# Performance work log

Hardware: AMD Instinct MI355X
Metric: run time of the kernel (lower is better)

The kernel has to match this reference:

```python
import jax, jax.numpy as jnp
import numpy as np

N_NODES = 100000
N_EDGES = 1000000
D_FEAT = 64
N_COARSE = 25000


def setup_inputs() -> dict:
    key = jax.random.key(0)
    k1, k2, k3 = jax.random.split(key, 3)
    x = jax.random.normal(k1, (N_NODES, D_FEAT), dtype=jnp.float32)
    edge_index = jax.random.randint(k2, (2, N_EDGES), 0, N_COARSE, dtype=jnp.int64)
    edge_attr = jax.random.uniform(k3, (N_EDGES,), dtype=jnp.float32)
    return {"x": x, "edge_index": edge_index, "edge_attr": edge_attr, "n_coarse": N_COARSE}


def reference(x, edge_index, edge_attr, n_coarse):
    # CustomPoolingAdd: for each edge e, out[dst[e]] += edge_attr[e] * x[src[e]]
    src = edge_index[0]  # [E]
    dst = edge_index[1]  # [E]
    msgs = x[src] * edge_attr[:, None]  # [E, D] gather + weight
    out = jax.ops.segment_sum(msgs, dst, num_segments=n_coarse)  # [n_coarse, D]
    return out
```

## Files before the change

kernel.cpp:

```cpp
#include <hip/hip_runtime.h>
#include <cmath>


constexpr int D4    = 16;
constexpr int NBSH  = 6;
constexpr int RPB   = 64;
constexpr int NB_LIM = 400;
constexpr int P1_C  = 3072;
constexpr int P1_K  = 19;
constexpr int CAPB  = 3072;

__global__ void __launch_bounds__(256) p1_bin_kernel(
    const int* __restrict__ src, const int* __restrict__ dst,
    const float* __restrict__ attr, int* __restrict__ cursor,
    int2* __restrict__ pairs, int n_edges, int nb) {
  __shared__ int2 bins[NB_LIM * P1_K];
  __shared__ int  bcnt[NB_LIM];
  __shared__ int  gbase_s[NB_LIM];
  for (int i = threadIdx.x; i < nb; i += 256) bcnt[i] = 0;
  __syncthreads();

  int base = blockIdx.x * P1_C;
  for (int i = threadIdx.x; i < P1_C; i += 256) {
    int e = base + i;
    if (e >= n_edges) break;
    int d = dst[e];
    int b = d >> NBSH;
    int2 pr = make_int2(src[e] | ((d & (RPB - 1)) << 24), __float_as_int(attr[e]));
    int p = atomicAdd(&bcnt[b], 1);
    if (p < P1_K) {
      bins[b * P1_K + p] = pr;
    } else {
      int g = atomicAdd(&cursor[b], 1);
      if (g < CAPB) pairs[(size_t)b * CAPB + g] = pr;
    }
  }
  __syncthreads();

  for (int b = threadIdx.x; b < nb; b += 256) {
    int c = min(bcnt[b], P1_K);
    gbase_s[b] = (c > 0) ? atomicAdd(&cursor[b], c) : 0;
  }
  __syncthreads();

  int wv = threadIdx.x >> 6, ln = threadIdx.x & 63;
  for (int b = wv; b < nb; b += 4) {
    int c = min(bcnt[b], P1_K);
    if (ln < c) {
      int g = gbase_s[b] + ln;
      if (g < CAPB) pairs[(size_t)b * CAPB + g] = bins[b * P1_K + ln];
    }
  }
}

__global__ void __launch_bounds__(512) p2_sort_kernel(
    const int* __restrict__ cursor, int2* __restrict__ pairs,
    int* __restrict__ row_off, int* __restrict__ row_cnt, int n_rows) {
  __shared__ int2 raw[CAPB];
  __shared__ int2 srt[CAPB];
  __shared__ int  cnt[RPB], off[RPB], cur[RPB];

  int b = blockIdx.x;
  int n = min(cursor[b], CAPB);
  size_t gbase = (size_t)b * CAPB;

  if (threadIdx.x < RPB) { cnt[threadIdx.x] = 0; cur[threadIdx.x] = 0; }
  __syncthreads();

  for (int i = threadIdx.x; i < n; i += 512) {
    int2 pr = pairs[gbase + i];
    raw[i] = pr;
    atomicAdd(&cnt[(pr.x >> 24) & (RPB - 1)], 1);
  }
  __syncthreads();

  if (threadIdx.x < RPB) {
    int c = cnt[threadIdx.x];
    int v = c;
    for (int d = 1; d < 64; d <<= 1) {
      int u = __shfl_up(v, d, 64);
      if (threadIdx.x >= d) v += u;
    }
    off[threadIdx.x] = v - c;
  }
  __syncthreads();

  for (int i = threadIdx.x; i < n; i += 512) {
    int2 pr = raw[i];
    int r = (pr.x >> 24) & (RPB - 1);
    int p = off[r] + atomicAdd(&cur[r], 1);
    srt[p] = make_int2(pr.x & 0xFFFFFF, pr.y);
  }
  __syncthreads();

  for (int i = threadIdx.x; i < n; i += 512)
    pairs[gbase + i] = srt[i];

  if (threadIdx.x < RPB) {
    int row = b * RPB + threadIdx.x;
    if (row < n_rows) {
      row_off[row] = (int)gbase + off[threadIdx.x];
      row_cnt[row] = cnt[threadIdx.x];
    }
  }
}

__global__ void __launch_bounds__(256) p3_gather_kernel(
    const float4* __restrict__ x4, const int* __restrict__ row_off,
    const int* __restrict__ row_cnt, const int2* __restrict__ pairs,
    float4* __restrict__ out4, int n_rows) {
  int wid = (blockIdx.x * blockDim.x + threadIdx.x) >> 6;
  if (wid >= n_rows) return;
  int lane = threadIdx.x & 63;
  int sub = lane >> 4;
  int q   = lane & 15;

  const int2* pb = pairs + row_off[wid];
  int n = row_cnt[wid];

  float4 a0 = make_float4(0.f,0.f,0.f,0.f), a1 = a0, a2 = a0, a3 = a0;
  int i = sub;
  for (; i + 12 < n; i += 16) {
    int2 p0 = pb[i];      int2 p1 = pb[i + 4];
    int2 p2 = pb[i + 8];  int2 p3 = pb[i + 12];
    float4 v0 = x4[(size_t)p0.x * D4 + q];
    float4 v1 = x4[(size_t)p1.x * D4 + q];
    float4 v2 = x4[(size_t)p2.x * D4 + q];
    float4 v3 = x4[(size_t)p3.x * D4 + q];
    float w0 = __int_as_float(p0.y), w1 = __int_as_float(p1.y);
    float w2 = __int_as_float(p2.y), w3 = __int_as_float(p3.y);
    a0.x += w0*v0.x; a0.y += w0*v0.y; a0.z += w0*v0.z; a0.w += w0*v0.w;
    a1.x += w1*v1.x; a1.y += w1*v1.y; a1.z += w1*v1.z; a1.w += w1*v1.w;
    a2.x += w2*v2.x; a2.y += w2*v2.y; a2.z += w2*v2.z; a2.w += w2*v2.w;
    a3.x += w3*v3.x; a3.y += w3*v3.y; a3.z += w3*v3.z; a3.w += w3*v3.w;
  }
  for (; i < n; i += 4) {
    int2 p0 = pb[i];
    float4 v0 = x4[(size_t)p0.x * D4 + q];
    float w0 = __int_as_float(p0.y);
    a0.x += w0*v0.x; a0.y += w0*v0.y; a0.z += w0*v0.z; a0.w += w0*v0.w;
  }
  a0.x += a1.x + a2.x + a3.x;
  a0.y += a1.y + a2.y + a3.y;
  a0.z += a1.z + a2.z + a3.z;
  a0.w += a1.w + a2.w + a3.w;
  for (int d = 16; d < 64; d <<= 1) {
    a0.x += __shfl_xor(a0.x, d, 64);
    a0.y += __shfl_xor(a0.y, d, 64);
    a0.z += __shfl_xor(a0.z, d, 64);
    a0.w += __shfl_xor(a0.w, d, 64);
  }
  if (sub == 0) out4[(size_t)wid * D4 + q] = a0;
}

__global__ void __launch_bounds__(256) scatter_cap_kernel(
    const int* __restrict__ src, const int* __restrict__ dst,
    const float* __restrict__ attr, int* __restrict__ cursor,
    int2* __restrict__ pairs, int n_edges, int cap) {
  int e = blockIdx.x * blockDim.x + threadIdx.x;
  if (e >= n_edges) return;
  int d = dst[e];
  int p = atomicAdd(&cursor[d], 1);
  if (p < cap) pairs[(size_t)d * cap + p] = make_int2(src[e], __float_as_int(attr[e]));
}

__global__ void __launch_bounds__(256) gather_cap_kernel(
    const float4* __restrict__ x4, const int* __restrict__ cnt,
    const int2* __restrict__ pairs, float4* __restrict__ out4,
    int n_rows, int cap) {
  int wid = (blockIdx.x * blockDim.x + threadIdx.x) >> 6;
  if (wid >= n_rows) return;
  int lane = threadIdx.x & 63;
  int sub = lane >> 4, q = lane & 15;
  int n = min(cnt[wid], cap);
  const int2* pb = pairs + (size_t)wid * cap;
  float4 a0 = make_float4(0.f,0.f,0.f,0.f), a1 = a0;
  int i = sub;
  for (; i + 4 < n; i += 8) {
    int2 p0 = pb[i]; int2 p1 = pb[i + 4];
    float4 v0 = x4[(size_t)p0.x * D4 + q];
    float4 v1 = x4[(size_t)p1.x * D4 + q];
    float w0 = __int_as_float(p0.y), w1 = __int_as_float(p1.y);
    a0.x += w0*v0.x; a0.y += w0*v0.y; a0.z += w0*v0.z; a0.w += w0*v0.w;
    a1.x += w1*v1.x; a1.y += w1*v1.y; a1.z += w1*v1.z; a1.w += w1*v1.w;
  }
  if (i < n) {
    int2 p0 = pb[i];
    float4 v0 = x4[(size_t)p0.x * D4 + q];
    float w0 = __int_as_float(p0.y);
    a0.x += w0*v0.x; a0.y += w0*v0.y; a0.z += w0*v0.z; a0.w += w0*v0.w;
  }
  a0.x += a1.x; a0.y += a1.y; a0.z += a1.z; a0.w += a1.w;
  for (int d = 16; d < 64; d <<= 1) {
    a0.x += __shfl_xor(a0.x, d, 64);
    a0.y += __shfl_xor(a0.y, d, 64);
    a0.z += __shfl_xor(a0.z, d, 64);
    a0.w += __shfl_xor(a0.w, d, 64);
  }
  if (sub == 0) out4[(size_t)wid * D4 + q] = a0;
}

__global__ void __launch_bounds__(256) scatter_add_kernel(
    const float4* __restrict__ x4, const int* __restrict__ src,
    const int* __restrict__ dst, const float* __restrict__ attr,
    float* __restrict__ out, int n_edges) {
  int t = blockIdx.x * blockDim.x + threadIdx.x;
  int e = t >> 4;
  if (e >= n_edges) return;
  int q = t & 15;
  float w = attr[e];
  float4 xv = x4[(size_t)src[e] * 16 + q];
  float* o = out + (size_t)dst[e] * 64 + q * 4;
  atomicAdd(o + 0, w * xv.x);
  atomicAdd(o + 1, w * xv.y);
  atomicAdd(o + 2, w * xv.z);
  atomicAdd(o + 3, w * xv.w);
}

static inline size_t align16(size_t v) { return (v + 15) & ~(size_t)15; }

extern "C" void kernel_launch(void* const* d_in, const int* in_sizes, int n_in,
                              void* d_out, int out_size, void* d_ws, size_t ws_size,
                              hipStream_t stream) {
  const float* x    = (const float*)d_in[0];
  const int*   ei   = (const int*)d_in[1];
  const float* attr = (const float*)d_in[2];
  float* out = (float*)d_out;

  const int n_edges = in_sizes[2];
  const int n_rows  = out_size / 64;
  const int* src = ei;
  const int* dst = ei + n_edges;

  const int nb = (n_rows + RPB - 1) >> NBSH;
  double lam = (double)n_edges / (nb > 0 ? nb : 1);
  bool shape_ok = (nb > 0) && (nb <= NB_LIM) &&
                  (lam + 8.0 * sqrt(lam) + 64.0 <= (double)CAPB);

  size_t cur_b  = align16((size_t)nb * 4);
  size_t roff_b = align16((size_t)n_rows * 4);
  size_t rcnt_b = align16((size_t)n_rows * 4);
  size_t need = cur_b + roff_b + rcnt_b + (size_t)nb * CAPB * 8;

  if (shape_ok && ws_size >= need) {
    int*  cursor  = (int*)d_ws;
    int*  row_off = (int*)((char*)d_ws + cur_b);
    int*  row_cnt = (int*)((char*)d_ws + cur_b + roff_b);
    int2* pairs   = (int2*)((char*)d_ws + cur_b + roff_b + rcnt_b);

    hipMemsetAsync(cursor, 0, (size_t)nb * 4, stream);

    int p1_grid = (n_edges + P1_C - 1) / P1_C;
    p1_bin_kernel<<<p1_grid, 256, 0, stream>>>(src, dst, attr, cursor, pairs,
                                               n_edges, nb);
    p2_sort_kernel<<<nb, 512, 0, stream>>>(cursor, pairs, row_off, row_cnt,
                                           n_rows);
    int p3_grid = (int)(((long long)n_rows * 64 + 255) / 256);
    p3_gather_kernel<<<p3_grid, 256, 0, stream>>>(
        (const float4*)x, row_off, row_cnt, pairs, (float4*)d_out, n_rows);
    return;
  }

  const int eb = (n_edges + 255) / 256;
  const int gb = (int)(((long long)n_rows * 64 + 255) / 256);
  size_t cb = align16((size_t)n_rows * 4);
  for (int cap : {128, 96}) {
    size_t need2 = cb + (size_t)n_rows * cap * 8;
    if (ws_size >= need2) {
      int* cursor = (int*)d_ws;
      int2* pairs = (int2*)((char*)d_ws + cb);
      hipMemsetAsync(cursor, 0, (size_t)n_rows * 4, stream);
      scatter_cap_kernel<<<eb, 256, 0, stream>>>(src, dst, attr, cursor, pairs,
                                                 n_edges, cap);
      gather_cap_kernel<<<gb, 256, 0, stream>>>(
          (const float4*)x, cursor, pairs, (float4*)d_out, n_rows, cap);
      return;
    }
  }

  hipMemsetAsync(d_out, 0, (size_t)out_size * sizeof(float), stream);
  long long threads = (long long)n_edges * 16;
  scatter_add_kernel<<<(int)((threads + 255) / 256), 256, 0, stream>>>(
      (const float4*)x, src, dst, attr, out, n_edges);
}
```

Measured before the change: 138.2 us.

## Fuse per-bin sort and gather into one LDS atomic accumulation kernel

Drops the per-bin counting sort and the separate per-row gather kernel. A single kernel per bin of 64 output rows now reads each binned (src,row,weight) entry, gathers the x row and accumulates into a shared-memory tile with float atomics, then writes the tile out. This removes one kernel launch, the sort pass over pairs and the row_off/row_cnt arrays. In exchange the gather runs in only one block per bin, which gives much less parallelism for the latency-bound x gather, adds LDS atomic contention, and makes the summation order nondeterministic.

```diff
diff --git a/kernel.cpp b/kernel.cpp
--- a/kernel.cpp
+++ b/kernel.cpp
@@ -53,104 +53,40 @@
   }
 }
 
-__global__ void __launch_bounds__(512) p2_sort_kernel(
-    const int* __restrict__ cursor, int2* __restrict__ pairs,
-    int* __restrict__ row_off, int* __restrict__ row_cnt, int n_rows) {
-  __shared__ int2 raw[CAPB];
-  __shared__ int2 srt[CAPB];
-  __shared__ int  cnt[RPB], off[RPB], cur[RPB];
+__global__ void __launch_bounds__(512) p2_acc_kernel(
+    const float4* __restrict__ x4, const int* __restrict__ cursor,
+    const int2* __restrict__ pairs, float4* __restrict__ out4, int n_rows) {
+  __shared__ float acc[RPB * 64];
 
   int b = blockIdx.x;
   int n = min(cursor[b], CAPB);
   size_t gbase = (size_t)b * CAPB;
 
-  if (threadIdx.x < RPB) { cnt[threadIdx.x] = 0; cur[threadIdx.x] = 0; }
-  __syncthreads();
-
-  for (int i = threadIdx.x; i < n; i += 512) {
+  for (int i = threadIdx.x; i < RPB * 64; i += 512) acc[i] = 0.f;
+  __syncthreads();
+
+  int sub = threadIdx.x >> 4;
+  int q   = threadIdx.x & 15;
+  for (int i = sub; i < n; i += 32) {
     int2 pr = pairs[gbase + i];
-    raw[i] = pr;
-    atomicAdd(&cnt[(pr.x >> 24) & (RPB - 1)], 1);
-  }
-  __syncthreads();
-
-  if (threadIdx.x < RPB) {
-    int c = cnt[threadIdx.x];
-    int v = c;
-    for (int d = 1; d < 64; d <<= 1) {
-      int u = __shfl_up(v, d, 64);
-      if (threadIdx.x >= d) v += u;
-    }
-    off[threadIdx.x] = v - c;
-  }
-  __syncthreads();
-
-  for (int i = threadIdx.x; i < n; i += 512) {
-    int2 pr = raw[i];
-    int r = (pr.x >> 24) & (RPB - 1);
-    int p = off[r] + atomicAdd(&cur[r], 1);
-    srt[p] = make_int2(pr.x & 0xFFFFFF, pr.y);
-  }
-  __syncthreads();
-
-  for (int i = threadIdx.x; i < n; i += 512)
-    pairs[gbase + i] = srt[i];
-
-  if (threadIdx.x < RPB) {
-    int row = b * RPB + threadIdx.x;
-    if (row < n_rows) {
-      row_off[row] = (int)gbase + off[threadIdx.x];
-      row_cnt[row] = cnt[threadIdx.x];
-    }
-  }
-}
-
-__global__ void __launch_bounds__(256) p3_gather_kernel(
-    const float4* __restrict__ x4, const int* __restrict__ row_off,
-    const int* __restrict__ row_cnt, const int2* __restrict__ pairs,
-    float4* __restrict__ out4, int n_rows) {
-  int wid = (blockIdx.x * blockDim.x + threadIdx.x) >> 6;
-  if (wid >= n_rows) return;
-  int lane = threadIdx.x & 63;
-  int sub = lane >> 4;
-  int q   = lane & 15;
-
-  const int2* pb = pairs + row_off[wid];
-  int n = row_cnt[wid];
-
-  float4 a0 = make_float4(0.f,0.f,0.f,0.f), a1 = a0, a2 = a0, a3 = a0;
-  int i = sub;
-  for (; i + 12 < n; i += 16) {
-    int2 p0 = pb[i];      int2 p1 = pb[i + 4];
-    int2 p2 = pb[i + 8];  int2 p3 = pb[i + 12];
-    float4 v0 = x4[(size_t)p0.x * D4 + q];
-    float4 v1 = x4[(size_t)p1.x * D4 + q];
-    float4 v2 = x4[(size_t)p2.x * D4 + q];
-    float4 v3 = x4[(size_t)p3.x * D4 + q];
-    float w0 = __int_as_float(p0.y), w1 = __int_as_float(p1.y);
-    float w2 = __int_as_float(p2.y), w3 = __int_as_float(p3.y);
-    a0.x += w0*v0.x; a0.y += w0*v0.y; a0.z += w0*v0.z; a0.w += w0*v0.w;
-    a1.x += w1*v1.x; a1.y += w1*v1.y; a1.z += w1*v1.z; a1.w += w1*v1.w;
-    a2.x += w2*v2.x; a2.y += w2*v2.y; a2.z += w2*v2.z; a2.w += w2*v2.w;
-    a3.x += w3*v3.x; a3.y += w3*v3.y; a3.z += w3*v3.z; a3.w += w3*v3.w;
-  }
-  for (; i < n; i += 4) {
-    int2 p0 = pb[i];
-    float4 v0 = x4[(size_t)p0.x * D4 + q];
-    float w0 = __int_as_float(p0.y);
-    a0.x += w0*v0.x; a0.y += w0*v0.y; a0.z += w0*v0.z; a0.w += w0*v0.w;
-  }
-  a0.x += a1.x + a2.x + a3.x;
-  a0.y += a1.y + a2.y + a3.y;
-  a0.z += a1.z + a2.z + a3.z;
-  a0.w += a1.w + a2.w + a3.w;
-  for (int d = 16; d < 64; d <<= 1) {
-    a0.x += __shfl_xor(a0.x, d, 64);
-    a0.y += __shfl_xor(a0.y, d, 64);
-    a0.z += __shfl_xor(a0.z, d, 64);
-    a0.w += __shfl_xor(a0.w, d, 64);
-  }
-  if (sub == 0) out4[(size_t)wid * D4 + q] = a0;
+    int row = (pr.x >> 24) & (RPB - 1);
+    float w = __int_as_float(pr.y);
+    float4 v = x4[(size_t)(pr.x & 0xFFFFFF) * D4 + q];
+    float* a = &acc[row * 64 + q * 4];
+    atomicAdd(a + 0, w * v.x);
+    atomicAdd(a + 1, w * v.y);
+    atomicAdd(a + 2, w * v.z);
+    atomicAdd(a + 3, w * v.w);
+  }
+  __syncthreads();
+
+  const float4* acc4 = (const float4*)acc;
+  int row0 = b * RPB;
+  for (int i = threadIdx.x; i < RPB * D4; i += 512) {
+    int row = i >> 4;
+    if (row0 + row < n_rows)
+      out4[(size_t)(row0 + row) * D4 + (i & (D4 - 1))] = acc4[i];
+  }
 }
 
 __global__ void __launch_bounds__(256) scatter_cap_kernel(
@@ -237,27 +173,20 @@
   bool shape_ok = (nb > 0) && (nb <= NB_LIM) &&
                   (lam + 8.0 * sqrt(lam) + 64.0 <= (double)CAPB);
 
-  size_t cur_b  = align16((size_t)nb * 4);
-  size_t roff_b = align16((size_t)n_rows * 4);
-  size_t rcnt_b = align16((size_t)n_rows * 4);
-  size_t need = cur_b + roff_b + rcnt_b + (size_t)nb * CAPB * 8;
+  size_t cur_b = align16((size_t)nb * 4);
+  size_t need = cur_b + (size_t)nb * CAPB * 8;
 
   if (shape_ok && ws_size >= need) {
-    int*  cursor  = (int*)d_ws;
-    int*  row_off = (int*)((char*)d_ws + cur_b);
-    int*  row_cnt = (int*)((char*)d_ws + cur_b + roff_b);
-    int2* pairs   = (int2*)((char*)d_ws + cur_b + roff_b + rcnt_b);
+    int*  cursor = (int*)d_ws;
+    int2* pairs  = (int2*)((char*)d_ws + cur_b);
 
     hipMemsetAsync(cursor, 0, (size_t)nb * 4, stream);
 
     int p1_grid = (n_edges + P1_C - 1) / P1_C;
     p1_bin_kernel<<<p1_grid, 256, 0, stream>>>(src, dst, attr, cursor, pairs,
                                                n_edges, nb);
-    p2_sort_kernel<<<nb, 512, 0, stream>>>(cursor, pairs, row_off, row_cnt,
-                                           n_rows);
-    int p3_grid = (int)(((long long)n_rows * 64 + 255) / 256);
-    p3_gather_kernel<<<p3_grid, 256, 0, stream>>>(
-        (const float4*)x, row_off, row_cnt, pairs, (float4*)d_out, n_rows);
+    p2_acc_kernel<<<nb, 512, 0, stream>>>(
+        (const float4*)x, cursor, pairs, (float4*)d_out, n_rows);
     return;
   }
 
```

New measurement: 536.2 us. 3.88x slower.
